# Performance work log

Measured on AMD Instinct MI355X. Metric: run time of the kernel, lower is better.

## Reference

```python
import jax, jax.numpy as jnp
import numpy as np

THRESH = 0.3
LENS = 0.5

@jax.custom_vjp
def spike_fn(x):
    return (x > 0).astype(x.dtype)

def _spike_fwd(x):
    return spike_fn(x), x

def _spike_bwd(x, g):
    # boxcar surrogate gradient: 1/(2*lens) for |x| < lens
    return (g * (jnp.abs(x) < LENS).astype(g.dtype) / (2.0 * LENS),)

spike_fn.defvjp(_spike_fwd, _spike_bwd)


def setup_inputs() -> dict:
    key = jax.random.key(0)
    ks = jax.random.split(key, 9)
    B, T, N_in, H, O = 256, 64, 700, 2048, 20
    s_ih = 1.0 / np.sqrt(N_in)
    s_hh = 1.0 / np.sqrt(H)
    s_ho = 1.0 / np.sqrt(H)
    return {
        "input": jax.random.uniform(ks[0], (B, T, N_in), dtype=jnp.float32),
        "W_ih": jax.random.normal(ks[1], (H, N_in), dtype=jnp.float32) * s_ih,
        "b_ih": jax.random.normal(ks[2], (H,), dtype=jnp.float32) * s_ih,
        "W_hh": jax.random.normal(ks[3], (H, H), dtype=jnp.float32) * s_hh,
        "b_hh": jax.random.normal(ks[4], (H,), dtype=jnp.float32) * s_hh,
        "W_ho": jax.random.normal(ks[5], (O, H), dtype=jnp.float32) * s_ho,
        "b_ho": jax.random.normal(ks[6], (O,), dtype=jnp.float32) * s_ho,
        "tau_m_h": jnp.full((1,), 20.0, dtype=jnp.float32),
        "tau_m_o": jnp.full((1,), 20.0, dtype=jnp.float32),
    }


def reference(input, W_ih, b_ih, W_hh, b_hh, W_ho, b_ho, tau_m_h, tau_m_o):
    B, T, _ = input.shape
    H = W_ih.shape[0]
    O = W_ho.shape[0]
    alpha_h = jnp.exp(-1.0 / tau_m_h)  # [1], broadcasts over [B, H]
    alpha_o = jnp.exp(-1.0 / tau_m_o)

    # Precompute input projection for all steps: [T, B, H]
    x_proj = jnp.einsum("bti,hi->tbh", input, W_ih) + b_ih

    def step(carry, xp):
        h_mem, h_spike, o_mem, o_spike, o_sum = carry
        # recurrent LIF hidden update
        h_mem = h_mem * alpha_h * (1.0 - h_spike) + xp + h_spike @ W_hh.T + b_hh
        h_spike = spike_fn(h_mem - THRESH)
        # output LIF update
        o_mem = o_mem * alpha_o * (1.0 - o_spike) + h_spike @ W_ho.T + b_ho
        o_spike = spike_fn(o_mem - THRESH)
        o_sum = o_sum + o_spike
        return (h_mem, h_spike, o_mem, o_spike, o_sum), None

    zH = jnp.zeros((B, H), dtype=input.dtype)
    zO = jnp.zeros((B, O), dtype=input.dtype)
    (_, _, _, _, o_sumspike), _ = jax.lax.scan(step, (zH, zH, zO, zO, zO), x_proj)
    return o_sumspike / T
```

## Files before the change

kernel.cpp:

```cpp
#include <hip/hip_runtime.h>
#include <stdint.h>

typedef __attribute__((ext_vector_type(4))) int i32x4;

static constexpr int BB = 256, TT = 64, NIN = 700, NKP = 768, HH = 2048, OO = 20;
static constexpr float THRESH_V = 0.3f;
static constexpr int NGEMM = 256;
static constexpr int NOB   = 1280;
static constexpr int NIT_REC = 16, NIT = 28;

static constexpr size_t OFF_HMEM  = 0;
static constexpr size_t OFF_SPK0  = 2097152;
static constexpr size_t OFF_OMEM  = 2621440;
static constexpr size_t OFF_OSPK  = 2641920;
static constexpr size_t OFF_OSUM  = 2662400;
static constexpr size_t ZERO_END  = 2682880;
static constexpr size_t OFF_SPK1  = 2682880;
static constexpr size_t OFF_ALPHA = 3207168;
static constexpr size_t OFF_WHHD  = 3207424;
static constexpr size_t WHH_PLANE = 4194304;
static constexpr size_t OFF_WIHD  = 19984640;
static constexpr size_t WIH_PLANE = 1572864;
static constexpr size_t OFF_XD    = 26276096;
static constexpr size_t XD_PLANE  = 12582912;
static constexpr size_t WS_NEED   = 76607744;

#define WAIT_VM6() asm volatile("s_waitcnt vmcnt(6)" ::: "memory")
#define WAIT_VM0() asm volatile("s_waitcnt vmcnt(0)" ::: "memory")
#define SCHED0()   __builtin_amdgcn_sched_barrier(0)

__device__ __forceinline__ void wdig(float w, double scale, signed char d[4]) {
    int q = (int)rint((double)w * scale);
    int t0 = (int)(signed char)(q & 0xFF); q = (q - t0) >> 8;
    int t1 = (int)(signed char)(q & 0xFF); q = (q - t1) >> 8;
    int t2 = (int)(signed char)(q & 0xFF); q = (q - t2) >> 8;
    d[0] = (signed char)t0; d[1] = (signed char)t1;
    d[2] = (signed char)t2; d[3] = (signed char)q;
}

__device__ __forceinline__ i32x4 ld_rec(const uint8_t* base, int row, int sl) {
    return *reinterpret_cast<const i32x4*>(base + row * 128 + ((sl ^ (row & 7)) << 4));
}
__device__ __forceinline__ i32x4 ld_x(const uint8_t* base, int row, int s) {
    int phys = (s + (row >> 1)) & 3;
    return *reinterpret_cast<const i32x4*>(base + row * 64 + (phys << 4));
}

__device__ __forceinline__ void gload(const uint8_t* src, uint8_t* dst) {
    __builtin_amdgcn_global_load_lds((const __attribute__((address_space(1))) void*)src,
                                     (__attribute__((address_space(3))) void*)dst, 16, 0, 0);
}

__device__ __forceinline__ void stage_rec(uint8_t* buf, const int8_t* spk, const int8_t* whhd,
                                          int m0, int n0, int k0B, int wid, int lane) {
#pragma unroll
    for (int i = 0; i < 2; ++i) {
        int c   = wid + i * 4;
        int row = c * 8 + (lane >> 3);
        int s   = (lane & 7) ^ (row & 7);
        gload((const uint8_t*)spk + (size_t)(m0 + row) * HH + k0B + (s << 4),
              buf + c * 1024);
    }
#pragma unroll
    for (int sub = 0; sub < 4; ++sub) {
        int row = sub * 8 + (lane >> 3);
        int s   = (lane & 7) ^ (row & 7);
        gload((const uint8_t*)whhd + (size_t)wid * WHH_PLANE +
              (size_t)(n0 + row) * HH + k0B + (s << 4),
              buf + 8192 + wid * 4096 + sub * 1024);
    }
}
__device__ __forceinline__ void stage_x(uint8_t* buf, const int8_t* xd_t, const int8_t* wihd,
                                        int m0, int n0, int k0B, int wid, int lane) {
#pragma unroll
    for (int sub = 0; sub < 4; ++sub) {
        int row = sub * 16 + (lane >> 2);
        int s   = ((lane & 3) - (row >> 1)) & 3;
        gload((const uint8_t*)xd_t + (size_t)wid * XD_PLANE +
              (size_t)(m0 + row) * NKP + k0B + (s << 4),
              buf + wid * 4096 + sub * 1024);
    }
#pragma unroll
    for (int i = 0; i < 2; ++i) {
        int cb  = wid + i * 4;
        int p   = cb >> 1, sub = cb & 1;
        int row = sub * 16 + (lane >> 2);
        int s   = ((lane & 3) - (row >> 1)) & 3;
        gload((const uint8_t*)wihd + (size_t)p * WIH_PLANE +
              (size_t)(n0 + row) * NKP + k0B + (s << 4),
              buf + 16384 + p * 2048 + sub * 1024);
    }
}

__device__ __forceinline__ void mfma_rec(const uint8_t* buf, int mw, int nw, int fr, int hi4,
                                         i32x4 aR[4][2]) {
#pragma unroll
    for (int ks = 0; ks < 2; ++ks) {
        int sl = ks * 4 + hi4;
        i32x4 a0 = ld_rec(buf, mw * 32 + fr,      sl);
        i32x4 a1 = ld_rec(buf, mw * 32 + 16 + fr, sl);
#pragma unroll
        for (int p = 0; p < 4; ++p) {
            i32x4 b = ld_rec(buf + 8192 + p * 4096, nw * 16 + fr, sl);
            aR[p][0] = __builtin_amdgcn_mfma_i32_16x16x64_i8(a0, b, aR[p][0], 0, 0, 0);
            aR[p][1] = __builtin_amdgcn_mfma_i32_16x16x64_i8(a1, b, aR[p][1], 0, 0, 0);
        }
    }
}
__device__ __forceinline__ void mfma_x(const uint8_t* buf, int mw, int nw, int fr, int hi4,
                                       i32x4 aX[5][2]) {
    i32x4 fa[4][2], fb[4];
#pragma unroll
    for (int p = 0; p < 4; ++p) {
        fa[p][0] = ld_x(buf + p * 4096, mw * 32 + fr,      hi4);
        fa[p][1] = ld_x(buf + p * 4096, mw * 32 + 16 + fr, hi4);
        fb[p]    = ld_x(buf + 16384 + p * 2048, nw * 16 + fr, hi4);
    }
#pragma unroll
    for (int a = 0; a < 4; ++a)
#pragma unroll
        for (int b = 0; b < 4; ++b) {
            if (a + b < 2) continue;
            const int c = a + b - 2;
            aX[c][0] = __builtin_amdgcn_mfma_i32_16x16x64_i8(fa[a][0], fb[b], aX[c][0], 0, 0, 0);
            aX[c][1] = __builtin_amdgcn_mfma_i32_16x16x64_i8(fa[a][1], fb[b], aX[c][1], 0, 0, 0);
        }
}

__global__ __launch_bounds__(256) void conv_whh_i8(const float* __restrict__ W,
                                                   int8_t* __restrict__ p0, int8_t* __restrict__ p1,
                                                   int8_t* __restrict__ p2, int8_t* __restrict__ p3,
                                                   const float* __restrict__ tau_h,
                                                   const float* __restrict__ tau_o,
                                                   float* __restrict__ alpha) {
    int idx = blockIdx.x * 256 + threadIdx.x;
    if (idx == 0) {
        float qh = __fdiv_rn(-1.0f, tau_h[0]);
        float qo = __fdiv_rn(-1.0f, tau_o[0]);
        alpha[0] = (float)exp((double)qh);
        alpha[1] = (float)exp((double)qo);
    }
    float4 v = reinterpret_cast<const float4*>(W)[idx];
    signed char dx[4], dy[4], dz[4], dw[4];
    const double SC = 1073741824.0;
    wdig(v.x, SC, dx); wdig(v.y, SC, dy); wdig(v.z, SC, dz); wdig(v.w, SC, dw);
    reinterpret_cast<char4*>(p0)[idx] = make_char4(dx[0], dy[0], dz[0], dw[0]);
    reinterpret_cast<char4*>(p1)[idx] = make_char4(dx[1], dy[1], dz[1], dw[1]);
    reinterpret_cast<char4*>(p2)[idx] = make_char4(dx[2], dy[2], dz[2], dw[2]);
    reinterpret_cast<char4*>(p3)[idx] = make_char4(dx[3], dy[3], dz[3], dw[3]);
}

__global__ __launch_bounds__(256) void conv_wih_i8(const float* __restrict__ W,
                                                   int8_t* __restrict__ p0, int8_t* __restrict__ p1,
                                                   int8_t* __restrict__ p2, int8_t* __restrict__ p3) {
    int row = blockIdx.x;
    for (int i = threadIdx.x; i < NKP; i += 256) {
        float v = (i < NIN) ? W[(size_t)row * NIN + i] : 0.f;
        signed char d[4];
        wdig(v, 1073741824.0, d);
        size_t o = (size_t)row * NKP + i;
        p0[o] = d[0]; p1[o] = d[1]; p2[o] = d[2]; p3[o] = d[3];
    }
}

__global__ __launch_bounds__(256) void conv_x_i8(const float* __restrict__ in,
                                                 int8_t* __restrict__ p0, int8_t* __restrict__ p1,
                                                 int8_t* __restrict__ p2, int8_t* __restrict__ p3) {
    int blk = blockIdx.x;
    int t = blk >> 8, b = blk & 255;
    const float* src = in + ((size_t)b * TT + t) * NIN;
    size_t dst = ((size_t)t * BB + b) * NKP;
    for (int i = threadIdx.x; i < NKP; i += 256) {
        float v = (i < NIN) ? src[i] : 0.f;
        signed char d[4];
        wdig(v, 16777216.0, d);
        p0[dst + i] = d[0]; p1[dst + i] = d[1]; p2[dst + i] = d[2]; p3[dst + i] = d[3];
    }
}

__device__ __forceinline__ void o_dot_wave(int pair, int lane, const int8_t* __restrict__ spk,
                                           const float* __restrict__ W_ho,
                                           const float* __restrict__ b_ho,
                                           float a_o, float* __restrict__ o_mem,
                                           float* __restrict__ o_spk, float* __restrict__ o_sum,
                                           float* __restrict__ out ) {
    int b = pair / OO, o = pair % OO;
    const int8_t* srow = spk  + (size_t)b * HH + lane * 32;
    const float*  wrow = W_ho + (size_t)o * HH + lane * 32;
    int4 s0 = *reinterpret_cast<const int4*>(srow);
    int4 s1 = *reinterpret_cast<const int4*>(srow + 16);
    int sw[8] = {s0.x, s0.y, s0.z, s0.w, s1.x, s1.y, s1.z, s1.w};
    double acc = 0.0;
#pragma unroll
    for (int q = 0; q < 8; ++q) {
        float4 w = *reinterpret_cast<const float4*>(wrow + q * 4);
        int sv = sw[q];
        acc += (sv & 0x000000FF) ? (double)w.x : 0.0;
        acc += (sv & 0x0000FF00) ? (double)w.y : 0.0;
        acc += (sv & 0x00FF0000) ? (double)w.z : 0.0;
        acc += (sv & 0xFF000000) ? (double)w.w : 0.0;
    }
#pragma unroll
    for (int off = 32; off >= 1; off >>= 1)
        acc += __shfl_xor(acc, off, 64);
    if (lane == 0) {
        float dot = (float)acc;
        size_t oo = (size_t)b * OO + o;
        float om = o_mem[oo], osp = o_spk[oo];
        float v = __fadd_rn(__fadd_rn(__fmul_rn(__fmul_rn(om, a_o), 1.f - osp), dot), b_ho[o]);
        float sn = (v > THRESH_V) ? 1.f : 0.f;
        o_mem[oo] = v;
        o_spk[oo] = sn;
        float s = __fadd_rn(o_sum[oo], sn);
        o_sum[oo] = s;
        if (out) out[oo] = __fmul_rn(s, 1.f / 64.f);
    }
}

__global__ __launch_bounds__(256, 2) void step_kernel(
    const int8_t* __restrict__ whhd, const int8_t* __restrict__ wihd,
    const int8_t* __restrict__ xd,
    const int8_t* __restrict__ spk_rd, int8_t* __restrict__ spk_wr,
    float* __restrict__ h_mem, const float* __restrict__ alpha,
    const float* __restrict__ b_ih, const float* __restrict__ b_hh,
    const float* __restrict__ W_ho, const float* __restrict__ b_ho,
    float* __restrict__ o_mem, float* __restrict__ o_spk, float* __restrict__ o_sum,
    int t) {
    __shared__ __align__(16) uint8_t L0[24576];
    __shared__ __align__(16) uint8_t L1[24576];
    __shared__ __align__(16) uint8_t L2[24576];

    int bid = blockIdx.x;
    int tid = threadIdx.x;
    int lane = tid & 63, wid = tid >> 6;

    if (bid < NGEMM) {
        int g = bid;
        int m0 = (g >> 6) * 64;
        int n0 = (g & 63) * 32;
        int mw = wid >> 1, nw = wid & 1;
        int fr = lane & 15, hi4 = lane >> 4;

        const int8_t* xd_t = xd + (size_t)t * BB * NKP;

        i32x4 aR[4][2] = {};
        i32x4 aX[5][2] = {};

        stage_rec(L0, spk_rd, whhd, m0, n0, 0,   wid, lane);
        stage_rec(L1, spk_rd, whhd, m0, n0, 128, wid, lane);

#pragma unroll
        for (int h = 0; h < NIT; ++h) {
            if (h < NIT - 1) { WAIT_VM6(); } else { WAIT_VM0(); }
            SCHED0();
            __builtin_amdgcn_s_barrier();
            if (h + 2 < NIT) {
                uint8_t* nb = ((h + 2) % 3 == 0) ? L0 : ((h + 2) % 3 == 1) ? L1 : L2;
                if (h + 2 < NIT_REC)
                    stage_rec(nb, spk_rd, whhd, m0, n0, (h + 2) * 128, wid, lane);
                else
                    stage_x(nb, xd_t, wihd, m0, n0, (h + 2 - NIT_REC) * 64, wid, lane);
            }
            const uint8_t* cb = (h % 3 == 0) ? L0 : (h % 3 == 1) ? L1 : L2;
            __builtin_amdgcn_s_setprio(1);
            if (h < NIT_REC) mfma_rec(cb, mw, nw, fr, hi4, aR);
            else             mfma_x(cb, mw, nw, fr, hi4, aX);
            __builtin_amdgcn_s_setprio(0);
        }

        float a_h = alpha[0];
        int j  = n0 + nw * 16 + fr;
        int rq = hi4 * 4;
#pragma unroll
        for (int msub = 0; msub < 2; ++msub)
#pragma unroll
            for (int r = 0; r < 4; ++r) {
                int b = m0 + mw * 32 + msub * 16 + rq + r;
                size_t off = (size_t)b * HH + j;
                float recf = (float)((double)aR[3][msub][r] * 0x1p-6
                                   + (double)aR[2][msub][r] * 0x1p-14
                                   + (double)aR[1][msub][r] * 0x1p-22
                                   + (double)aR[0][msub][r] * 0x1p-30);
                double xp64 = (double)aX[4][msub][r] * 0x1p-6
                            + (double)aX[3][msub][r] * 0x1p-14
                            + (double)aX[2][msub][r] * 0x1p-22
                            + (double)aX[1][msub][r] * 0x1p-30
                            + (double)aX[0][msub][r] * 0x1p-38;
                float xpf = (float)xp64;
                float xpb = __fadd_rn(xpf, b_ih[j]);
                float hv  = h_mem[off];
                float keep = spk_rd[off] ? 0.f : 1.f;
                float v = __fadd_rn(__fmul_rn(__fmul_rn(hv, a_h), keep), xpb);
                v = __fadd_rn(v, recf);
                v = __fadd_rn(v, b_hh[j]);
                h_mem[off] = v;
                spk_wr[off] = (v > THRESH_V) ? (int8_t)1 : (int8_t)0;
            }
    } else {
        if (t == 0) return;
        int pair = (bid - NGEMM) * 4 + wid;
        o_dot_wave(pair, lane, spk_rd, W_ho, b_ho, alpha[1], o_mem, o_spk, o_sum, nullptr);
    }
}

__global__ __launch_bounds__(256) void final_kernel(const int8_t* __restrict__ spk,
                                                    const float* __restrict__ W_ho,
                                                    const float* __restrict__ b_ho,
                                                    const float* __restrict__ alpha,
                                                    float* __restrict__ o_mem,
                                                    float* __restrict__ o_spk,
                                                    float* __restrict__ o_sum,
                                                    float* __restrict__ out) {
    int lane = threadIdx.x & 63, wid = threadIdx.x >> 6;
    int pair = blockIdx.x * 4 + wid;
    o_dot_wave(pair, lane, spk, W_ho, b_ho, alpha[1], o_mem, o_spk, o_sum, out);
}

extern "C" void kernel_launch(void* const* d_in, const int* in_sizes, int n_in,
                              void* d_out, int out_size, void* d_ws, size_t ws_size,
                              hipStream_t stream) {
    const float* in    = (const float*)d_in[0];
    const float* W_ih  = (const float*)d_in[1];
    const float* b_ih  = (const float*)d_in[2];
    const float* W_hh  = (const float*)d_in[3];
    const float* b_hh  = (const float*)d_in[4];
    const float* W_ho  = (const float*)d_in[5];
    const float* b_ho  = (const float*)d_in[6];
    const float* tau_h = (const float*)d_in[7];
    const float* tau_o = (const float*)d_in[8];

    uint8_t* ws = (uint8_t*)d_ws;
    float*  h_mem = (float*)(ws + OFF_HMEM);
    int8_t* spk0  = (int8_t*)(ws + OFF_SPK0);
    float*  o_mem = (float*)(ws + OFF_OMEM);
    float*  o_spk = (float*)(ws + OFF_OSPK);
    float*  o_sum = (float*)(ws + OFF_OSUM);
    int8_t* spk1  = (int8_t*)(ws + OFF_SPK1);
    float*  alpha = (float*)(ws + OFF_ALPHA);
    int8_t* whhd  = (int8_t*)(ws + OFF_WHHD);
    int8_t* wihd  = (int8_t*)(ws + OFF_WIHD);
    int8_t* xd    = (int8_t*)(ws + OFF_XD);

    if (ws_size < WS_NEED) return;

    hipMemsetAsync(ws, 0, ZERO_END, stream);
    conv_whh_i8<<<4096, 256, 0, stream>>>(W_hh,
                                          whhd, whhd + WHH_PLANE, whhd + 2 * WHH_PLANE, whhd + 3 * WHH_PLANE,
                                          tau_h, tau_o, alpha);
    conv_wih_i8<<<2048, 256, 0, stream>>>(W_ih,
                                          wihd, wihd + WIH_PLANE, wihd + 2 * WIH_PLANE, wihd + 3 * WIH_PLANE);
    conv_x_i8<<<16384, 256, 0, stream>>>(in,
                                         xd, xd + XD_PLANE, xd + 2 * XD_PLANE, xd + 3 * XD_PLANE);

    for (int t = 0; t < TT; ++t) {
        const int8_t* srd = (t & 1) ? spk1 : spk0;
        int8_t*       swr = (t & 1) ? spk0 : spk1;
        step_kernel<<<NGEMM + NOB, 256, 0, stream>>>(whhd, wihd, xd, srd, swr, h_mem, alpha,
                                                     b_ih, b_hh, W_ho, b_ho,
                                                     o_mem, o_spk, o_sum, t);
    }
    final_kernel<<<NOB, 256, 0, stream>>>(spk0, W_ho, b_ho, alpha, o_mem, o_spk, o_sum,
                                          (float*)d_out);
}
```

Before: 1.365 ms.

## Hoist input projection into a batched kernel and deepen recurrent pipeline

Moves the input-projection GEMM for all timesteps out of the per-step kernel into one batched xproj_kernel, which writes fp32 projections to a new workspace buffer. The per-step kernel now runs only the recurrent GEMM and reads the precomputed projection. Its LDS ring grows to four stages with a prefetch depth of three, and the occupancy hint is dropped. The aim is to shorten the serial per-step critical path, at the cost of a 128MB extra buffer plus one big upfront launch, and lower occupancy from 96KB of LDS.

```diff
diff --git a/kernel.cpp b/kernel.cpp
--- a/kernel.cpp
+++ b/kernel.cpp
@@ -7,7 +7,8 @@
 static constexpr float THRESH_V = 0.3f;
 static constexpr int NGEMM = 256;
 static constexpr int NOB   = 1280;
-static constexpr int NIT_REC = 16, NIT = 28;
+static constexpr int NREC  = 16;
+static constexpr int XNIT  = 12;
 
 static constexpr size_t OFF_HMEM  = 0;
 static constexpr size_t OFF_SPK0  = 2097152;
@@ -23,11 +24,13 @@
 static constexpr size_t WIH_PLANE = 1572864;
 static constexpr size_t OFF_XD    = 26276096;
 static constexpr size_t XD_PLANE  = 12582912;
-static constexpr size_t WS_NEED   = 76607744;
-
-#define WAIT_VM6() asm volatile("s_waitcnt vmcnt(6)" ::: "memory")
-#define WAIT_VM0() asm volatile("s_waitcnt vmcnt(0)" ::: "memory")
-#define SCHED0()   __builtin_amdgcn_sched_barrier(0)
+static constexpr size_t OFF_XP    = 76607744;
+static constexpr size_t WS_NEED   = 210825472;
+
+#define WAIT_VM12() asm volatile("s_waitcnt vmcnt(12)" ::: "memory")
+#define WAIT_VM6()  asm volatile("s_waitcnt vmcnt(6)" ::: "memory")
+#define WAIT_VM0()  asm volatile("s_waitcnt vmcnt(0)" ::: "memory")
+#define SCHED0()    __builtin_amdgcn_sched_barrier(0)
 
 __device__ __forceinline__ void wdig(float w, double scale, signed char d[4]) {
     int q = (int)rint((double)w * scale);
@@ -176,6 +179,59 @@
         wdig(v, 16777216.0, d);
         p0[dst + i] = d[0]; p1[dst + i] = d[1]; p2[dst + i] = d[2]; p3[dst + i] = d[3];
     }
+}
+
+__global__ __launch_bounds__(256, 2) void xproj_kernel(const int8_t* __restrict__ xd,
+                                                       const int8_t* __restrict__ wihd,
+                                                       float* __restrict__ xp) {
+    __shared__ __align__(16) uint8_t X0[24576];
+    __shared__ __align__(16) uint8_t X1[24576];
+    __shared__ __align__(16) uint8_t X2[24576];
+
+    int bid = blockIdx.x;
+    int n0 = (bid & 63) * 32;
+    int m0 = ((bid >> 6) & 3) * 64;
+    int t  = bid >> 8;
+    int tid = threadIdx.x;
+    int lane = tid & 63, wid = tid >> 6;
+    int mw = wid >> 1, nw = wid & 1;
+    int fr = lane & 15, hi4 = lane >> 4;
+
+    const int8_t* xd_t = xd + (size_t)t * BB * NKP;
+    i32x4 aX[5][2] = {};
+
+    stage_x(X0, xd_t, wihd, m0, n0, 0,  wid, lane);
+    stage_x(X1, xd_t, wihd, m0, n0, 64, wid, lane);
+#pragma unroll
+    for (int j = 0; j < XNIT; ++j) {
+        if (j <= XNIT - 2) { WAIT_VM6(); } else { WAIT_VM0(); }
+        SCHED0();
+        __builtin_amdgcn_s_barrier();
+        if (j + 2 < XNIT) {
+            uint8_t* nb = ((j + 2) % 3 == 0) ? X0 : ((j + 2) % 3 == 1) ? X1 : X2;
+            stage_x(nb, xd_t, wihd, m0, n0, (j + 2) * 64, wid, lane);
+        }
+        const uint8_t* cb = (j % 3 == 0) ? X0 : (j % 3 == 1) ? X1 : X2;
+        __builtin_amdgcn_s_setprio(1);
+        mfma_x(cb, mw, nw, fr, hi4, aX);
+        __builtin_amdgcn_s_setprio(0);
+    }
+
+    int jcol = n0 + nw * 16 + fr;
+    int rq = hi4 * 4;
+    float* xp_t = xp + (size_t)t * BB * HH;
+#pragma unroll
+    for (int msub = 0; msub < 2; ++msub)
+#pragma unroll
+        for (int r = 0; r < 4; ++r) {
+            int b = m0 + mw * 32 + msub * 16 + rq + r;
+            double xp64 = (double)aX[4][msub][r] * 0x1p-6
+                        + (double)aX[3][msub][r] * 0x1p-14
+                        + (double)aX[2][msub][r] * 0x1p-22
+                        + (double)aX[1][msub][r] * 0x1p-30
+                        + (double)aX[0][msub][r] * 0x1p-38;
+            xp_t[(size_t)b * HH + jcol] = (float)xp64;
+        }
 }
 
 __device__ __forceinline__ void o_dot_wave(int pair, int lane, const int8_t* __restrict__ spk,
@@ -217,9 +273,8 @@
     }
 }
 
-__global__ __launch_bounds__(256, 2) void step_kernel(
-    const int8_t* __restrict__ whhd, const int8_t* __restrict__ wihd,
-    const int8_t* __restrict__ xd,
+__global__ __launch_bounds__(256) void step_kernel(
+    const int8_t* __restrict__ whhd, const float* __restrict__ xp,
     const int8_t* __restrict__ spk_rd, int8_t* __restrict__ spk_wr,
     float* __restrict__ h_mem, const float* __restrict__ alpha,
     const float* __restrict__ b_ih, const float* __restrict__ b_hh,
@@ -229,46 +284,45 @@
     __shared__ __align__(16) uint8_t L0[24576];
     __shared__ __align__(16) uint8_t L1[24576];
     __shared__ __align__(16) uint8_t L2[24576];
+    __shared__ __align__(16) uint8_t L3[24576];
 
     int bid = blockIdx.x;
     int tid = threadIdx.x;
     int lane = tid & 63, wid = tid >> 6;
 
     if (bid < NGEMM) {
-        int g = bid;
-        int m0 = (g >> 6) * 64;
-        int n0 = (g & 63) * 32;
+        int m0 = (bid >> 6) * 64;
+        int n0 = (bid & 63) * 32;
         int mw = wid >> 1, nw = wid & 1;
         int fr = lane & 15, hi4 = lane >> 4;
 
-        const int8_t* xd_t = xd + (size_t)t * BB * NKP;
-
         i32x4 aR[4][2] = {};
-        i32x4 aX[5][2] = {};
 
         stage_rec(L0, spk_rd, whhd, m0, n0, 0,   wid, lane);
         stage_rec(L1, spk_rd, whhd, m0, n0, 128, wid, lane);
-
-#pragma unroll
-        for (int h = 0; h < NIT; ++h) {
-            if (h < NIT - 1) { WAIT_VM6(); } else { WAIT_VM0(); }
+        stage_rec(L2, spk_rd, whhd, m0, n0, 256, wid, lane);
+
+#pragma unroll
+        for (int h = 0; h < NREC; ++h) {
+            if (h <= NREC - 3) { WAIT_VM12(); }
+            else if (h == NREC - 2) { WAIT_VM6(); }
+            else { WAIT_VM0(); }
             SCHED0();
             __builtin_amdgcn_s_barrier();
-            if (h + 2 < NIT) {
-                uint8_t* nb = ((h + 2) % 3 == 0) ? L0 : ((h + 2) % 3 == 1) ? L1 : L2;
-                if (h + 2 < NIT_REC)
-                    stage_rec(nb, spk_rd, whhd, m0, n0, (h + 2) * 128, wid, lane);
-                else
-                    stage_x(nb, xd_t, wihd, m0, n0, (h + 2 - NIT_REC) * 64, wid, lane);
+            if (h + 3 < NREC) {
+                uint8_t* nb = ((h + 3) & 3) == 0 ? L0 : ((h + 3) & 3) == 1 ? L1
+                            : ((h + 3) & 3) == 2 ? L2 : L3;
+                stage_rec(nb, spk_rd, whhd, m0, n0, (h + 3) * 128, wid, lane);
             }
-            const uint8_t* cb = (h % 3 == 0) ? L0 : (h % 3 == 1) ? L1 : L2;
+            const uint8_t* cb = (h & 3) == 0 ? L0 : (h & 3) == 1 ? L1
+                              : (h & 3) == 2 ? L2 : L3;
             __builtin_amdgcn_s_setprio(1);
-            if (h < NIT_REC) mfma_rec(cb, mw, nw, fr, hi4, aR);
-            else             mfma_x(cb, mw, nw, fr, hi4, aX);
+            mfma_rec(cb, mw, nw, fr, hi4, aR);
             __builtin_amdgcn_s_setprio(0);
         }
 
         float a_h = alpha[0];
+        const float* xp_t = xp + (size_t)t * BB * HH;
         int j  = n0 + nw * 16 + fr;
         int rq = hi4 * 4;
 #pragma unroll
@@ -281,12 +335,7 @@
                                    + (double)aR[2][msub][r] * 0x1p-14
                                    + (double)aR[1][msub][r] * 0x1p-22
                                    + (double)aR[0][msub][r] * 0x1p-30);
-                double xp64 = (double)aX[4][msub][r] * 0x1p-6
-                            + (double)aX[3][msub][r] * 0x1p-14
-                            + (double)aX[2][msub][r] * 0x1p-22
-                            + (double)aX[1][msub][r] * 0x1p-30
-                            + (double)aX[0][msub][r] * 0x1p-38;
-                float xpf = (float)xp64;
+                float xpf = xp_t[off];
                 float xpb = __fadd_rn(xpf, b_ih[j]);
                 float hv  = h_mem[off];
                 float keep = spk_rd[off] ? 0.f : 1.f;
@@ -340,6 +389,7 @@
     int8_t* whhd  = (int8_t*)(ws + OFF_WHHD);
     int8_t* wihd  = (int8_t*)(ws + OFF_WIHD);
     int8_t* xd    = (int8_t*)(ws + OFF_XD);
+    float*  xp    = (float*)(ws + OFF_XP);
 
     if (ws_size < WS_NEED) return;
 
@@ -351,11 +401,12 @@
                                           wihd, wihd + WIH_PLANE, wihd + 2 * WIH_PLANE, wihd + 3 * WIH_PLANE);
     conv_x_i8<<<16384, 256, 0, stream>>>(in,
                                          xd, xd + XD_PLANE, xd + 2 * XD_PLANE, xd + 3 * XD_PLANE);
+    xproj_kernel<<<16384, 256, 0, stream>>>(xd, wihd, xp);
 
     for (int t = 0; t < TT; ++t) {
         const int8_t* srd = (t & 1) ? spk1 : spk0;
         int8_t*       swr = (t & 1) ? spk0 : spk1;
-        step_kernel<<<NGEMM + NOB, 256, 0, stream>>>(whhd, wihd, xd, srd, swr, h_mem, alpha,
+        step_kernel<<<NGEMM + NOB, 256, 0, stream>>>(whhd, xp, srd, swr, h_mem, alpha,
                                                      b_ih, b_hh, W_ho, b_ho,
                                                      o_mem, o_spk, o_sum, t);
     }
```

Result: slower. 1.691 ms (+23.9%).

## Deepen LDS prefetch pipeline, drop padded K tile, fold output dot into GEMM blocks

Applied to the files above, without the earlier changes.

The per-step GEMM loop moves from three to four LDS buffers with a prefetch distance of three, waiting on vmcnt(12), so more global loads are in flight. The input-projection loop drops its last K tile, which only covers zero padding (700 real columns, padded to 768). The separate 1280 output-dot blocks are removed: each of the 256 GEMM blocks now computes the 20 output neurons for one batch row after its hidden update. This cuts grid size and launch work, but runs the output dot serially at the tail of every block. The extra 24 KB of LDS and the dropped min-blocks launch bound may lower occupancy.

```diff
diff --git a/kernel.cpp b/kernel.cpp
--- a/kernel.cpp
+++ b/kernel.cpp
@@ -5,9 +5,10 @@
 
 static constexpr int BB = 256, TT = 64, NIN = 700, NKP = 768, HH = 2048, OO = 20;
 static constexpr float THRESH_V = 0.3f;
-static constexpr int NGEMM = 256;
-static constexpr int NOB   = 1280;
-static constexpr int NIT_REC = 16, NIT = 28;
+static constexpr int NBLK = 256;
+static constexpr int NREC = 16;
+static constexpr int XNIT = 11;
+static constexpr int NIT  = NREC + XNIT;
 
 static constexpr size_t OFF_HMEM  = 0;
 static constexpr size_t OFF_SPK0  = 2097152;
@@ -24,10 +25,10 @@
 static constexpr size_t OFF_XD    = 26276096;
 static constexpr size_t XD_PLANE  = 12582912;
 static constexpr size_t WS_NEED   = 76607744;
-
-#define WAIT_VM6() asm volatile("s_waitcnt vmcnt(6)" ::: "memory")
-#define WAIT_VM0() asm volatile("s_waitcnt vmcnt(0)" ::: "memory")
-#define SCHED0()   __builtin_amdgcn_sched_barrier(0)
+#define WAIT_VM12() asm volatile("s_waitcnt vmcnt(12)" ::: "memory")
+#define WAIT_VM6()  asm volatile("s_waitcnt vmcnt(6)" ::: "memory")
+#define WAIT_VM0()  asm volatile("s_waitcnt vmcnt(0)" ::: "memory")
+#define SCHED0()    __builtin_amdgcn_sched_barrier(0)
 
 __device__ __forceinline__ void wdig(float w, double scale, signed char d[4]) {
     int q = (int)rint((double)w * scale);
@@ -178,46 +179,49 @@
     }
 }
 
-__device__ __forceinline__ void o_dot_wave(int pair, int lane, const int8_t* __restrict__ spk,
+__device__ __forceinline__ void odot_block(int g, int wid, int lane, const int8_t* __restrict__ spk,
                                            const float* __restrict__ W_ho,
                                            const float* __restrict__ b_ho,
                                            float a_o, float* __restrict__ o_mem,
                                            float* __restrict__ o_spk, float* __restrict__ o_sum,
                                            float* __restrict__ out ) {
-    int b = pair / OO, o = pair % OO;
-    const int8_t* srow = spk  + (size_t)b * HH + lane * 32;
-    const float*  wrow = W_ho + (size_t)o * HH + lane * 32;
+    const int8_t* srow = spk + (size_t)g * HH + lane * 32;
     int4 s0 = *reinterpret_cast<const int4*>(srow);
     int4 s1 = *reinterpret_cast<const int4*>(srow + 16);
     int sw[8] = {s0.x, s0.y, s0.z, s0.w, s1.x, s1.y, s1.z, s1.w};
-    double acc = 0.0;
-#pragma unroll
-    for (int q = 0; q < 8; ++q) {
-        float4 w = *reinterpret_cast<const float4*>(wrow + q * 4);
-        int sv = sw[q];
-        acc += (sv & 0x000000FF) ? (double)w.x : 0.0;
-        acc += (sv & 0x0000FF00) ? (double)w.y : 0.0;
-        acc += (sv & 0x00FF0000) ? (double)w.z : 0.0;
-        acc += (sv & 0xFF000000) ? (double)w.w : 0.0;
-    }
-#pragma unroll
-    for (int off = 32; off >= 1; off >>= 1)
-        acc += __shfl_xor(acc, off, 64);
-    if (lane == 0) {
-        float dot = (float)acc;
-        size_t oo = (size_t)b * OO + o;
-        float om = o_mem[oo], osp = o_spk[oo];
-        float v = __fadd_rn(__fadd_rn(__fmul_rn(__fmul_rn(om, a_o), 1.f - osp), dot), b_ho[o]);
-        float sn = (v > THRESH_V) ? 1.f : 0.f;
-        o_mem[oo] = v;
-        o_spk[oo] = sn;
-        float s = __fadd_rn(o_sum[oo], sn);
-        o_sum[oo] = s;
-        if (out) out[oo] = __fmul_rn(s, 1.f / 64.f);
-    }
-}
-
-__global__ __launch_bounds__(256, 2) void step_kernel(
+#pragma unroll 1
+    for (int p = 0; p < 5; ++p) {
+        int o = wid * 5 + p;
+        const float* wrow = W_ho + (size_t)o * HH + lane * 32;
+        double acc = 0.0;
+#pragma unroll
+        for (int q = 0; q < 8; ++q) {
+            float4 w = *reinterpret_cast<const float4*>(wrow + q * 4);
+            int sv = sw[q];
+            acc += (sv & 0x000000FF) ? (double)w.x : 0.0;
+            acc += (sv & 0x0000FF00) ? (double)w.y : 0.0;
+            acc += (sv & 0x00FF0000) ? (double)w.z : 0.0;
+            acc += (sv & 0xFF000000) ? (double)w.w : 0.0;
+        }
+#pragma unroll
+        for (int off = 32; off >= 1; off >>= 1)
+            acc += __shfl_xor(acc, off, 64);
+        if (lane == 0) {
+            float dot = (float)acc;
+            size_t oo = (size_t)g * OO + o;
+            float om = o_mem[oo], osp = o_spk[oo];
+            float v = __fadd_rn(__fadd_rn(__fmul_rn(__fmul_rn(om, a_o), 1.f - osp), dot), b_ho[o]);
+            float sn = (v > THRESH_V) ? 1.f : 0.f;
+            o_mem[oo] = v;
+            o_spk[oo] = sn;
+            float s = __fadd_rn(o_sum[oo], sn);
+            o_sum[oo] = s;
+            if (out) out[oo] = __fmul_rn(s, 1.f / 64.f);
+        }
+    }
+}
+
+__global__ __launch_bounds__(256) void step_kernel(
     const int8_t* __restrict__ whhd, const int8_t* __restrict__ wihd,
     const int8_t* __restrict__ xd,
     const int8_t* __restrict__ spk_rd, int8_t* __restrict__ spk_wr,
@@ -229,78 +233,78 @@
     __shared__ __align__(16) uint8_t L0[24576];
     __shared__ __align__(16) uint8_t L1[24576];
     __shared__ __align__(16) uint8_t L2[24576];
-
-    int bid = blockIdx.x;
+    __shared__ __align__(16) uint8_t L3[24576];
+
+    int g   = blockIdx.x;
     int tid = threadIdx.x;
     int lane = tid & 63, wid = tid >> 6;
-
-    if (bid < NGEMM) {
-        int g = bid;
-        int m0 = (g >> 6) * 64;
-        int n0 = (g & 63) * 32;
-        int mw = wid >> 1, nw = wid & 1;
-        int fr = lane & 15, hi4 = lane >> 4;
-
-        const int8_t* xd_t = xd + (size_t)t * BB * NKP;
-
-        i32x4 aR[4][2] = {};
-        i32x4 aX[5][2] = {};
-
-        stage_rec(L0, spk_rd, whhd, m0, n0, 0,   wid, lane);
-        stage_rec(L1, spk_rd, whhd, m0, n0, 128, wid, lane);
-
-#pragma unroll
-        for (int h = 0; h < NIT; ++h) {
-            if (h < NIT - 1) { WAIT_VM6(); } else { WAIT_VM0(); }
-            SCHED0();
-            __builtin_amdgcn_s_barrier();
-            if (h + 2 < NIT) {
-                uint8_t* nb = ((h + 2) % 3 == 0) ? L0 : ((h + 2) % 3 == 1) ? L1 : L2;
-                if (h + 2 < NIT_REC)
-                    stage_rec(nb, spk_rd, whhd, m0, n0, (h + 2) * 128, wid, lane);
-                else
-                    stage_x(nb, xd_t, wihd, m0, n0, (h + 2 - NIT_REC) * 64, wid, lane);
-            }
-            const uint8_t* cb = (h % 3 == 0) ? L0 : (h % 3 == 1) ? L1 : L2;
-            __builtin_amdgcn_s_setprio(1);
-            if (h < NIT_REC) mfma_rec(cb, mw, nw, fr, hi4, aR);
-            else             mfma_x(cb, mw, nw, fr, hi4, aX);
-            __builtin_amdgcn_s_setprio(0);
-        }
-
-        float a_h = alpha[0];
-        int j  = n0 + nw * 16 + fr;
-        int rq = hi4 * 4;
-#pragma unroll
-        for (int msub = 0; msub < 2; ++msub)
-#pragma unroll
-            for (int r = 0; r < 4; ++r) {
-                int b = m0 + mw * 32 + msub * 16 + rq + r;
-                size_t off = (size_t)b * HH + j;
-                float recf = (float)((double)aR[3][msub][r] * 0x1p-6
-                                   + (double)aR[2][msub][r] * 0x1p-14
-                                   + (double)aR[1][msub][r] * 0x1p-22
-                                   + (double)aR[0][msub][r] * 0x1p-30);
-                double xp64 = (double)aX[4][msub][r] * 0x1p-6
-                            + (double)aX[3][msub][r] * 0x1p-14
-                            + (double)aX[2][msub][r] * 0x1p-22
-                            + (double)aX[1][msub][r] * 0x1p-30
-                            + (double)aX[0][msub][r] * 0x1p-38;
-                float xpf = (float)xp64;
-                float xpb = __fadd_rn(xpf, b_ih[j]);
-                float hv  = h_mem[off];
-                float keep = spk_rd[off] ? 0.f : 1.f;
-                float v = __fadd_rn(__fmul_rn(__fmul_rn(hv, a_h), keep), xpb);
-                v = __fadd_rn(v, recf);
-                v = __fadd_rn(v, b_hh[j]);
-                h_mem[off] = v;
-                spk_wr[off] = (v > THRESH_V) ? (int8_t)1 : (int8_t)0;
-            }
-    } else {
-        if (t == 0) return;
-        int pair = (bid - NGEMM) * 4 + wid;
-        o_dot_wave(pair, lane, spk_rd, W_ho, b_ho, alpha[1], o_mem, o_spk, o_sum, nullptr);
-    }
+    int m0 = (g >> 6) * 64;
+    int n0 = (g & 63) * 32;
+    int mw = wid >> 1, nw = wid & 1;
+    int fr = lane & 15, hi4 = lane >> 4;
+
+    const int8_t* xd_t = xd + (size_t)t * BB * NKP;
+
+    i32x4 aR[4][2] = {};
+    i32x4 aX[5][2] = {};
+
+    stage_rec(L0, spk_rd, whhd, m0, n0, 0,   wid, lane);
+    stage_rec(L1, spk_rd, whhd, m0, n0, 128, wid, lane);
+    stage_rec(L2, spk_rd, whhd, m0, n0, 256, wid, lane);
+
+#pragma unroll
+    for (int h = 0; h < NIT; ++h) {
+        if (h <= NIT - 3) { WAIT_VM12(); }
+        else if (h == NIT - 2) { WAIT_VM6(); }
+        else { WAIT_VM0(); }
+        SCHED0();
+        __builtin_amdgcn_s_barrier();
+        if (h + 3 < NIT) {
+            uint8_t* nb = ((h + 3) & 3) == 0 ? L0 : ((h + 3) & 3) == 1 ? L1
+                        : ((h + 3) & 3) == 2 ? L2 : L3;
+            int c = h + 3;
+            if (c < NREC) stage_rec(nb, spk_rd, whhd, m0, n0, c * 128, wid, lane);
+            else          stage_x(nb, xd_t, wihd, m0, n0, (c - NREC) * 64, wid, lane);
+        }
+        const uint8_t* cb = (h & 3) == 0 ? L0 : (h & 3) == 1 ? L1
+                          : (h & 3) == 2 ? L2 : L3;
+        __builtin_amdgcn_s_setprio(1);
+        if (h < NREC) mfma_rec(cb, mw, nw, fr, hi4, aR);
+        else          mfma_x(cb, mw, nw, fr, hi4, aX);
+        __builtin_amdgcn_s_setprio(0);
+    }
+
+    float a_h = alpha[0];
+    int j  = n0 + nw * 16 + fr;
+    int rq = hi4 * 4;
+#pragma unroll
+    for (int msub = 0; msub < 2; ++msub)
+#pragma unroll
+        for (int rr = 0; rr < 4; ++rr) {
+            int b = m0 + mw * 32 + msub * 16 + rq + rr;
+            size_t off = (size_t)b * HH + j;
+            float recf = (float)((double)aR[3][msub][rr] * 0x1p-6
+                               + (double)aR[2][msub][rr] * 0x1p-14
+                               + (double)aR[1][msub][rr] * 0x1p-22
+                               + (double)aR[0][msub][rr] * 0x1p-30);
+            double xp64 = (double)aX[4][msub][rr] * 0x1p-6
+                        + (double)aX[3][msub][rr] * 0x1p-14
+                        + (double)aX[2][msub][rr] * 0x1p-22
+                        + (double)aX[1][msub][rr] * 0x1p-30
+                        + (double)aX[0][msub][rr] * 0x1p-38;
+            float xpf = (float)xp64;
+            float xpb = __fadd_rn(xpf, b_ih[j]);
+            float hv  = h_mem[off];
+            float keep = spk_rd[off] ? 0.f : 1.f;
+            float v = __fadd_rn(__fmul_rn(__fmul_rn(hv, a_h), keep), xpb);
+            v = __fadd_rn(v, recf);
+            v = __fadd_rn(v, b_hh[j]);
+            h_mem[off] = v;
+            spk_wr[off] = (v > THRESH_V) ? (int8_t)1 : (int8_t)0;
+        }
+
+    if (t > 0)
+        odot_block(g, wid, lane, spk_rd, W_ho, b_ho, alpha[1], o_mem, o_spk, o_sum, nullptr);
 }
 
 __global__ __launch_bounds__(256) void final_kernel(const int8_t* __restrict__ spk,
@@ -312,8 +316,7 @@
                                                     float* __restrict__ o_sum,
                                                     float* __restrict__ out) {
     int lane = threadIdx.x & 63, wid = threadIdx.x >> 6;
-    int pair = blockIdx.x * 4 + wid;
-    o_dot_wave(pair, lane, spk, W_ho, b_ho, alpha[1], o_mem, o_spk, o_sum, out);
+    odot_block(blockIdx.x, wid, lane, spk, W_ho, b_ho, alpha[1], o_mem, o_spk, o_sum, out);
 }
 
 extern "C" void kernel_launch(void* const* d_in, const int* in_sizes, int n_in,
@@ -355,10 +358,10 @@
     for (int t = 0; t < TT; ++t) {
         const int8_t* srd = (t & 1) ? spk1 : spk0;
         int8_t*       swr = (t & 1) ? spk0 : spk1;
-        step_kernel<<<NGEMM + NOB, 256, 0, stream>>>(whhd, wihd, xd, srd, swr, h_mem, alpha,
-                                                     b_ih, b_hh, W_ho, b_ho,
-                                                     o_mem, o_spk, o_sum, t);
-    }
-    final_kernel<<<NOB, 256, 0, stream>>>(spk0, W_ho, b_ho, alpha, o_mem, o_spk, o_sum,
-                                          (float*)d_out);
-}
+        step_kernel<<<NBLK, 256, 0, stream>>>(whhd, wihd, xd, srd, swr, h_mem, alpha,
+                                              b_ih, b_hh, W_ho, b_ho,
+                                              o_mem, o_spk, o_sum, t);
+    }
+    final_kernel<<<NBLK, 256, 0, stream>>>(spk0, W_ho, b_ho, alpha, o_mem, o_spk, o_sum,
+                                           (float*)d_out);
+}
```

New measurement: 1.541 ms. 1.13x slower.
